# Kernel optimization log

Hardware: AMD Instinct MI355X
Metric: run time of the kernel (lower is better)

Reference implementation:

```python
import jax, jax.numpy as jnp
import numpy as np

N_STATES = 8
LBW = 128          # look_back_window == seq_len L (required by the einsum)
PRED_W = 16        # prediction_window
C = 16             # look_back_channel_dim
B = 512
LOG2PI = float(np.log(2.0 * np.pi))


def setup_inputs() -> dict:
    key = jax.random.key(0)
    k0, k1, k2, k3, k4 = jax.random.split(key, 5)
    emissions = jax.random.normal(k0, (B, LBW, C), jnp.float32)
    transition_matrix = jax.random.normal(k1, (N_STATES, N_STATES), jnp.float32)
    initial_distribution = jax.random.normal(k2, (N_STATES,), jnp.float32)
    means = jax.random.normal(k3, (N_STATES, C), jnp.float32)
    covar_chol = jnp.tile(jnp.eye(C, dtype=jnp.float32)[None], (N_STATES, 1, 1))
    W = jax.random.normal(k4, (N_STATES, LBW, C, C), jnp.float32) * 0.01
    return {"emissions": emissions, "transition_matrix": transition_matrix,
            "initial_distribution": initial_distribution, "means": means,
            "covar_chol": covar_chol, "W": W}


def reference(emissions, transition_matrix, initial_distribution, means, covar_chol, W):
    Bs, L, Cc = emissions.shape
    S = means.shape[0]
    lbw = W.shape[1]

    # --- positive-definite covariances from Cholesky factors (exp on diagonal) ---
    d = jnp.diagonal(covar_chol, axis1=-2, axis2=-1)                 # (S, C)
    chol = jnp.tril(covar_chol, -1) + jax.vmap(jnp.diag)(jnp.exp(d)) # (S, C, C)
    covar = chol @ jnp.swapaxes(chol, -1, -2) + 1e-6 * jnp.eye(Cc, dtype=emissions.dtype)
    prec = jnp.linalg.inv(covar)                                     # (S, C, C)
    Lc = jnp.linalg.cholesky(covar)
    logdet = 2.0 * jnp.sum(jnp.log(jnp.diagonal(Lc, axis1=-2, axis2=-1)), axis=-1)  # (S,)

    # --- per-step Gaussian log-likelihood with linear AR mean ---
    # causal zero-padded history: window f, element l = padded[f + l]
    padded = jnp.concatenate([jnp.zeros_like(emissions), emissions], axis=1)  # (B, 2L, C)
    idx = jnp.arange(L)[:, None] + jnp.arange(L)[None, :]                     # (L, L)
    inputs = padded[:, idx, :]                                                # (B, L, L, C)
    ar = jnp.einsum('bflc,slcd->bsfd', inputs, W)                             # (B, S, L, C)
    diff = emissions[:, None] - (ar + means[None, :, None])                   # (B, S, L, C)
    quad = jnp.einsum('bslc,scd,bsld->bsl', diff, prec, diff)                 # (B, S, L)
    emis_ll = -0.5 * (quad + logdet[None, :, None] + Cc * LOG2PI)
    emis_ll = jnp.transpose(emis_ll, (0, 2, 1))                               # (B, L, S)

    # --- HMM forward algorithm (log-space scan over time) ---
    log_trans = jnp.log(jax.nn.softmax(transition_matrix, axis=1) + 1e-8)     # (S, S)
    la0 = jnp.log(jax.nn.softmax(initial_distribution)) + emis_ll[:, 0]       # (B, S)

    def step(la, e_t):
        la = jax.nn.logsumexp(la[:, :, None] + log_trans[None], axis=1) + e_t
        return la, None

    la_last, _ = jax.lax.scan(step, la0, jnp.transpose(emis_ll[:, 1:], (1, 0, 2)))

    trans = jax.nn.softmax(transition_matrix, axis=1)
    state = jnp.argmax(la_last, axis=1)                                       # (B,)
    buf = emissions[:, -lbw:]                                                 # (B, lbw, C)
    preds = []
    for _ in range(PRED_W):
        state = jnp.argmax(trans[state], axis=1)
        pred = jnp.einsum('blc,blcd->bd', buf, W[state]) + means[state]       # (B, C)
        preds.append(pred)
        buf = jnp.concatenate([buf[:, 1:], pred[:, None]], axis=1)
    return jnp.stack(preds, axis=1)                                           # (B, PRED_W, C)
```

## Files before the change

kernel.cpp:

```cpp
#include <hip/hip_runtime.h>
#include <hip/hip_bf16.h>

#define LOG2PI_F 1.8378770664093453f
#define LOG2E_F  1.44269504f

typedef float f32x4 __attribute__((ext_vector_type(4)));
typedef short s16x8 __attribute__((ext_vector_type(8)));
typedef unsigned short u16;

#define OFF_PREC   0
#define OFF_LOGDET 2048
#define OFF_LTR    2064
#define OFF_LINI   2128
#define OFF_CHAIN  2144
#define OFF_CNT    2272
#define OFF_PERM   2304
#define OFF_ELL    8192
#define OFF_WT     532480

__device__ inline u16 f2bf(float x) {
  union { float f; unsigned u; } v; v.f = x;
  unsigned r = v.u + 0x7fffu + ((v.u >> 16) & 1u);
  return (u16)(r >> 16);
}

__device__ inline float fexp2(float x) {
#if __has_builtin(__builtin_amdgcn_exp2f)
  return __builtin_amdgcn_exp2f(x);
#else
  return exp2f(x);
#endif
}
__device__ inline float flog2(float x) {
#if __has_builtin(__builtin_amdgcn_logf)
  return __builtin_amdgcn_logf(x);
#else
  return log2f(x);
#endif
}

__global__ __launch_bounds__(256) void prep_wt_kernel(const float* __restrict__ tmat,
                                                      const float* __restrict__ initd,
                                                      const float* __restrict__ cc,
                                                      const float* __restrict__ W,
                                                      float* __restrict__ ws) {
  __shared__ float Ls[8][16][16];
  __shared__ float tmp[256];
  int t = threadIdx.x;

  if (blockIdx.x < 1024) {
    u16* Wt = (u16*)(ws + OFF_WT);
    int sl = blockIdx.x;
    tmp[t] = W[sl * 256 + t];
    __syncthreads();
    int d = t >> 4, c = t & 15;
    Wt[sl * 256 + t] = f2bf(tmp[c * 16 + d]);
    return;
  }

  float* prec   = ws + OFF_PREC;
  float* logdet = ws + OFF_LOGDET;
  float* ltr    = ws + OFF_LTR;
  float* lini   = ws + OFF_LINI;
  int*   chain  = (int*)(ws + OFF_CHAIN);

  if (t < 128) {
    int s = t >> 4, i = t & 15;
    const float* c0 = cc + s * 256 + i * 16;
    for (int j = 0; j < 16; ++j) {
      float v = c0[j];
      Ls[s][i][j] = (i > j) ? v : (i == j ? expf(v) : 0.f);
    }
  } else if (t < 136) {
    int s = t - 128;
    float ld = 0.f;
    for (int i = 0; i < 16; ++i) ld += cc[s * 256 + i * 17];
    logdet[s] = 2.f * ld;
  } else if (t == 136) {
    float m = -1e30f;
    for (int i = 0; i < 8; ++i) m = fmaxf(m, initd[i]);
    float sum = 0.f;
    for (int i = 0; i < 8; ++i) sum += expf(initd[i] - m);
    float lsum = logf(sum);
    for (int i = 0; i < 8; ++i) lini[i] = (initd[i] - m - lsum) * LOG2E_F;
  } else if (t == 137) {
    int nxt[8];
    for (int i = 0; i < 8; ++i) {
      float best = -1e30f; int bi = 0;
      for (int j = 0; j < 8; ++j) {
        float v = tmat[i * 8 + j];
        if (v > best) { best = v; bi = j; }
      }
      nxt[i] = bi;
    }
    for (int s0 = 0; s0 < 8; ++s0) {
      int c = s0;
      for (int k = 0; k < 16; ++k) { c = nxt[c]; chain[s0 * 16 + k] = c; }
    }
  } else if (t == 138) {
    int* cnt = (int*)(ws + OFF_CNT);
    for (int i = 0; i < 8; ++i) cnt[i] = 0;
  } else if (t >= 144 && t < 152) {
    int i = t - 144;
    float m = -1e30f;
    for (int j = 0; j < 8; ++j) m = fmaxf(m, tmat[i * 8 + j]);
    float sum = 0.f;
    for (int j = 0; j < 8; ++j) sum += expf(tmat[i * 8 + j] - m);
    for (int j = 0; j < 8; ++j)
      ltr[i * 8 + j] = logf(expf(tmat[i * 8 + j] - m) / sum + 1e-8f) * LOG2E_F;
  }
  __syncthreads();
  if (t < 128) {
    int s = t >> 4, col = t & 15;
    float y[16], x[16];
#pragma unroll
    for (int i = 0; i < 16; ++i) {
      float v = (i == col) ? 1.f : 0.f;
#pragma unroll
      for (int k = 0; k < 16; ++k) if (k < i) v -= Ls[s][i][k] * y[k];
      y[i] = v / Ls[s][i][i];
    }
#pragma unroll
    for (int i = 15; i >= 0; --i) {
      float v = y[i];
#pragma unroll
      for (int k = 0; k < 16; ++k) if (k > i) v -= Ls[s][k][i] * x[k];
      x[i] = v / Ls[s][i][i];
    }
#pragma unroll
    for (int i = 0; i < 16; ++i) prec[s * 256 + i * 16 + col] = x[i];
  }
}

__global__ __launch_bounds__(512, 4) void emis_kernel(const float* __restrict__ emis,
                                                      const float* __restrict__ means,
                                                      float* __restrict__ ws) {
  const float* prec   = ws + OFF_PREC;
  const float* logdet = ws + OFF_LOGDET;
  const u16* Wt = (const u16*)(ws + OFF_WT);
  float* ell = ws + OFF_ELL;

  int sp = blockIdx.x & 3;
  int bg = blockIdx.x >> 2;
  int s0 = sp * 2;
  int bb0 = bg * 4;
  int tid = threadIdx.x;

  __shared__ __align__(16) char smem[40960];
  char* pbase = smem;
  float* dlf = (float*)smem;
  const s16x8 zero8 = {0, 0, 0, 0, 0, 0, 0, 0};

  for (int i = tid; i < 1024; i += 512)
    *(s16x8*)(pbase + (i >> 8) * 8192 + (i & 255) * 16) = zero8;
  for (int i = tid; i < 1024; i += 512) {
    int g = i >> 8, erow = (i >> 1) & 127, h2 = i & 1;
    const f32x4* src = (const f32x4*)(emis + (size_t)(bb0 + g) * 2048 + erow * 16 + h2 * 8);
    f32x4 v0 = src[0], v1 = src[1];
    s16x8 pk;
#pragma unroll
    for (int c = 0; c < 4; ++c) { pk[c] = (short)f2bf(v0[c]); pk[c + 4] = (short)f2bf(v1[c]); }
    int row = 128 + erow;
    int off = ((row << 5) + (h2 << 4)) ^ (((row >> 2) & 3) << 4);
    *(s16x8*)(pbase + g * 8192 + off) = pk;
  }
  __syncthreads();

  int wave = tid >> 6, lane = tid & 63;
  int mt = (wave < 4) ? wave : 11 - wave;
  int rc = lane & 15;
  int h  = (lane >> 4) & 1;
  int dl = lane >> 5;
  int hh = h << 4;
  int kst = 56 - 8 * mt;
  int r0 = mt * 16 + rc + dl;

  const u16* Bp0 = Wt + ((size_t)((s0 * 128 + dl) * 16 + rc) * 16) + h * 8 + (size_t)kst * 512;
  const u16* Bp1 = Bp0 + 32768;

  f32x4 acc[2][4] = {};
  s16x8 w0 = *(const s16x8*)Bp0, w1 = *(const s16x8*)Bp1;
  for (int kk = kst; kk < 64; ++kk) {
    s16x8 n0, n1;
    if (kk < 63) { n0 = *(const s16x8*)(Bp0 + 512); n1 = *(const s16x8*)(Bp1 + 512); }
    Bp0 += 512; Bp1 += 512;
    int row = r0 + 2 * kk;
    const char* pa = pbase + (((row << 5) + hh) ^ (((row >> 2) & 3) << 4));
#pragma unroll
    for (int g = 0; g < 4; ++g) {
      s16x8 a = *(const s16x8*)(pa + g * 8192);
      acc[0][g] = __builtin_amdgcn_mfma_f32_16x16x32_bf16(a, w0, acc[0][g], 0, 0, 0);
      acc[1][g] = __builtin_amdgcn_mfma_f32_16x16x32_bf16(a, w1, acc[1][g], 0, 0, 0);
    }
    w0 = n0; w1 = n1;
  }

  int hi = (lane >> 4) & 3;
  float ev[4][4];
#pragma unroll
  for (int g = 0; g < 4; ++g)
#pragma unroll
    for (int r = 0; r < 4; ++r)
      ev[g][r] = emis[(size_t)(bb0 + g) * 2048 + (mt * 16 + hi * 4 + r) * 16 + rc];

  __syncthreads();

#pragma unroll
  for (int s = 0; s < 2; ++s) {
    float mn = means[(s0 + s) * 16 + rc];
#pragma unroll
    for (int g = 0; g < 4; ++g) {
#pragma unroll
      for (int r = 0; r < 4; ++r) {
        int f = mt * 16 + hi * 4 + r;
        dlf[(g * 128 + f) * 20 + rc] = ev[g][r] - acc[s][g][r] - mn;
      }
    }
    __syncthreads();
    const float* P = prec + (s0 + s) * 256;
    float c2 = -0.72134752f * (logdet[s0 + s] + 16.f * LOG2PI_F);
    {
      int g = tid >> 7, f = tid & 127;
      float dv[16];
#pragma unroll
      for (int c = 0; c < 4; ++c)
        *(f32x4*)&dv[c * 4] = *(const f32x4*)&dlf[(g * 128 + f) * 20 + c * 4];
      float qq = 0.f;
#pragma unroll
      for (int c = 0; c < 16; ++c) {
        float tsum = 0.5f * P[c * 16 + c] * dv[c];
#pragma unroll
        for (int d2 = 0; d2 < 16; ++d2)
          if (d2 > c) tsum = fmaf(P[c * 16 + d2], dv[d2], tsum);
        qq = fmaf(dv[c], tsum, qq);
      }
      ell[((size_t)(bb0 + g) * 8 + s0 + s) * 128 + f] = fmaf(-2.f * 0.72134752f, qq, c2);
    }
    if (s == 0) __syncthreads();
  }
}

__global__ __launch_bounds__(256) void fwd_kernel(float* __restrict__ ws) {
  const float* ell  = ws + OFF_ELL;
  const float* ltr  = ws + OFF_LTR;
  const float* lini = ws + OFF_LINI;
  int* cnt  = (int*)(ws + OFF_CNT);
  int* perm = (int*)(ws + OFF_PERM);

  __shared__ float leaf[8192];
  __shared__ float lvl[4096];
  __shared__ float ebuf[1024];
  __shared__ float LTs[64];
  __shared__ float redv[8];

  int b = blockIdx.x, tid = threadIdx.x;

  *(f32x4*)&ebuf[tid * 4] = *(const f32x4*)(ell + (size_t)b * 1024 + tid * 4);
  if (tid < 64) LTs[tid] = ltr[tid];
  __syncthreads();

  for (int t = tid; t < 8192; t += 256) {
    int m = t >> 6, i = (t >> 3) & 7, j = t & 7;
    float v;
    if (m < 127) v = LTs[i * 8 + j] + ebuf[j * 128 + (m + 1)];
    else         v = (i == j) ? 0.f : -1e30f;
    leaf[t] = v;
  }
  __syncthreads();

  float* src = leaf;
  float* dst = lvl;
  int nm = 64;
  for (int level = 0; level < 7; ++level) {
    for (int t = tid; t < nm * 64; t += 256) {
      int p = t >> 6, i = (t >> 3) & 7, j = t & 7;
      const float* Ma = src + (p * 2) * 64 + i * 8;
      const float* Mb = src + (p * 2 + 1) * 64 + j;
      float sv[8];
#pragma unroll
      for (int k = 0; k < 8; ++k) sv[k] = Ma[k] + Mb[k * 8];
      float m01 = fmaxf(sv[0], sv[1]), m23 = fmaxf(sv[2], sv[3]);
      float m45 = fmaxf(sv[4], sv[5]), m67 = fmaxf(sv[6], sv[7]);
      float m = fmaxf(fmaxf(m01, m23), fmaxf(m45, m67));
      float sum = ((fexp2(sv[0] - m) + fexp2(sv[1] - m))
                 + (fexp2(sv[2] - m) + fexp2(sv[3] - m)))
                + ((fexp2(sv[4] - m) + fexp2(sv[5] - m))
                 + (fexp2(sv[6] - m) + fexp2(sv[7] - m)));
      dst[p * 64 + i * 8 + j] = m + flog2(sum);
    }
    __syncthreads();
    float* tswap = src; src = dst; dst = tswap;
    nm >>= 1;
  }

  if (tid < 8) {
    int s = tid;
    float sv[8];
#pragma unroll
    for (int i = 0; i < 8; ++i)
      sv[i] = lini[i] + ebuf[i * 128] + src[i * 8 + s];
    float m01 = fmaxf(sv[0], sv[1]), m23 = fmaxf(sv[2], sv[3]);
    float m45 = fmaxf(sv[4], sv[5]), m67 = fmaxf(sv[6], sv[7]);
    float m = fmaxf(fmaxf(m01, m23), fmaxf(m45, m67));
    float sum = ((fexp2(sv[0] - m) + fexp2(sv[1] - m))
               + (fexp2(sv[2] - m) + fexp2(sv[3] - m)))
              + ((fexp2(sv[4] - m) + fexp2(sv[5] - m))
               + (fexp2(sv[6] - m) + fexp2(sv[7] - m)));
    redv[s] = m + flog2(sum);
  }
  __syncthreads();
  if (tid == 0) {
    float best = -1e30f; int bi = 0;
#pragma unroll
    for (int i = 0; i < 8; ++i) {
      float o = redv[i];
      if (o > best) { best = o; bi = i; }
    }
    int pos = atomicAdd(&cnt[bi], 1);
    perm[bi * 512 + pos] = b;
  }
}

__global__ __launch_bounds__(512, 2) void pred_kernel(const float* __restrict__ emis,
                                                      const float* __restrict__ means,
                                                      float* __restrict__ ws,
                                                      float* __restrict__ out) {
  const int* chain = (const int*)(ws + OFF_CHAIN);
  const int* cnt   = (const int*)(ws + OFF_CNT);
  const int* perm  = (const int*)(ws + OFF_PERM);
  const u16* Wt = (const u16*)(ws + OFF_WT);

  __shared__ u16 buf[16][128][16];
  __shared__ float part[8][64][4];
  __shared__ float ms[8][16];
  __shared__ int bid[16];

  int bucket = blockIdx.x >> 5, slot = blockIdx.x & 31;
  int nb = cnt[bucket];
  int base = slot * 16;
  if (base >= nb) return;
  int tid = threadIdx.x;
  char* pb = (char*)&buf[0][0][0];

  if (tid < 16) {
    int idx = base + tid;
    bid[tid] = perm[bucket * 512 + (idx < nb ? idx : base)];
  } else if (tid >= 128 && tid < 256) {
    int t2 = tid - 128;
    ms[t2 >> 4][t2 & 15] = means[t2];
  }
  __syncthreads();

  for (int i = tid; i < 2048; i += 512) {
    int b = i >> 7, row = i & 127;
    const f32x4* sp = (const f32x4*)(emis + (size_t)bid[b] * 2048 + row * 16);
    f32x4 v0 = sp[0], v1 = sp[1], v2 = sp[2], v3 = sp[3];
    s16x8 p0, p1;
#pragma unroll
    for (int j = 0; j < 4; ++j) {
      p0[j] = (short)f2bf(v0[j]); p0[4 + j] = (short)f2bf(v1[j]);
      p1[j] = (short)f2bf(v2[j]); p1[4 + j] = (short)f2bf(v3[j]);
    }
    int xo = (b & 7) << 4;
    int bse = b * 4096 + row * 32;
    *(s16x8*)(pb + (bse ^ xo)) = p0;
    *(s16x8*)(pb + ((bse + 16) ^ xo)) = p1;
  }
  __syncthreads();

  int wave = tid >> 6, lane = tid & 63;
  int rc = lane & 15;
  int q  = lane >> 4;
  int h  = q & 1;
  int dl = q >> 1;
  int axor = (rc & 7) << 4;
  const int* mychain = chain + bucket * 16;
  int b_own = q * 4 + (wave & 3);
  int bown_base = b_own * 4096;
  int bown_xor = (b_own & 7) << 4;

  float outv[16];
  int start = 0;
#pragma unroll
  for (int k = 0; k < 16; ++k) {
    int st = mychain[k];
    const u16* Bb = Wt + ((size_t)((st * 128 + dl) * 16 + rc) * 16) + h * 8;
    f32x4 accA = {0.f, 0.f, 0.f, 0.f}, accB = {0.f, 0.f, 0.f, 0.f};
#pragma unroll
    for (int t2 = 0; t2 < 4; ++t2) {
      int kkA = wave * 8 + t2 * 2, kkB = kkA + 1;
      s16x8 wA = *(const s16x8*)(Bb + (size_t)kkA * 512);
      s16x8 wB2 = *(const s16x8*)(Bb + (size_t)kkB * 512);
      int rowA = (start + kkA * 2 + dl) & 127;
      int rowB = (start + kkB * 2 + dl) & 127;
      s16x8 aA = *(const s16x8*)(pb + ((rc * 4096 + rowA * 32 + h * 16) ^ axor));
      s16x8 aB = *(const s16x8*)(pb + ((rc * 4096 + rowB * 32 + h * 16) ^ axor));
      accA = __builtin_amdgcn_mfma_f32_16x16x32_bf16(aA, wA, accA, 0, 0, 0);
      accB = __builtin_amdgcn_mfma_f32_16x16x32_bf16(aB, wB2, accB, 0, 0, 0);
    }
    f32x4 acc = accA + accB;
    *(f32x4*)&part[wave][lane][0] = acc;
    __syncthreads();
    if (wave < 4) {
      f32x4 cs = (*(f32x4*)&part[0][lane][0] + *(f32x4*)&part[1][lane][0])
               + (*(f32x4*)&part[2][lane][0] + *(f32x4*)&part[3][lane][0]);
      f32x4 cs2 = (*(f32x4*)&part[4][lane][0] + *(f32x4*)&part[5][lane][0])
                + (*(f32x4*)&part[6][lane][0] + *(f32x4*)&part[7][lane][0]);
      cs = cs + cs2;
      float vown = (wave & 3) == 0 ? cs[0] : (wave & 3) == 1 ? cs[1]
                 : (wave & 3) == 2 ? cs[2] : cs[3];
      float o = vown + ms[st][rc];
      outv[k] = o;
      *(u16*)(pb + ((bown_base + start * 32 + rc * 2) ^ bown_xor)) = f2bf(o);
    }
    __syncthreads();
    start = (start + 1) & 127;
  }
  if (wave < 4 && base + b_own < nb) {
    float* op = out + (size_t)bid[b_own] * 256 + rc;
#pragma unroll
    for (int k = 0; k < 16; ++k) op[k * 16] = outv[k];
  }
}

extern "C" void kernel_launch(void* const* d_in, const int* in_sizes, int n_in,
                              void* d_out, int out_size, void* d_ws, size_t ws_size,
                              hipStream_t stream) {
  const float* emis  = (const float*)d_in[0];
  const float* tmat  = (const float*)d_in[1];
  const float* initd = (const float*)d_in[2];
  const float* means = (const float*)d_in[3];
  const float* cc    = (const float*)d_in[4];
  const float* W     = (const float*)d_in[5];
  float* ws  = (float*)d_ws;
  float* out = (float*)d_out;

  hipLaunchKernelGGL(prep_wt_kernel, dim3(1025), dim3(256), 0, stream, tmat, initd, cc, W, ws);
  hipLaunchKernelGGL(emis_kernel, dim3(512), dim3(512), 0, stream, emis, means, ws);
  hipLaunchKernelGGL(fwd_kernel, dim3(512), dim3(256), 0, stream, ws);
  hipLaunchKernelGGL(pred_kernel, dim3(256), dim3(512), 0, stream, emis, means, ws, out);
}
```

Measured before the change: 74.06 us.

## Switch forward tree reduction to scaled linear-space matmul; halve pred_kernel block size

The forward algorithm's log-space tree of 8x8 log-sum-exp matrix products becomes linear-space products. Leaves are exponentiated once after subtracting a per-step max, and each product is renormalised by its max across the wave. This removes the exp/log work per element at each of the seven levels. Separately, pred_kernel moves from 8 waves to 4, so each wave does twice the MFMA chain and the cross-wave reduction shrinks. Risks are precision loss from rescaling only by the per-product max and less parallelism in the prediction stage.

Result: slower. 82.13 us (+10.9%).

```diff
diff --git a/kernel.cpp b/kernel.cpp
--- a/kernel.cpp
+++ b/kernel.cpp
@@ -29,13 +29,6 @@
   return __builtin_amdgcn_exp2f(x);
 #else
   return exp2f(x);
-#endif
-}
-__device__ inline float flog2(float x) {
-#if __has_builtin(__builtin_amdgcn_logf)
-  return __builtin_amdgcn_logf(x);
-#else
-  return log2f(x);
 #endif
 }
 
@@ -251,19 +244,32 @@
   __shared__ float lvl[4096];
   __shared__ float ebuf[1024];
   __shared__ float LTs[64];
+  __shared__ float kmax[128];
   __shared__ float redv[8];
 
   int b = blockIdx.x, tid = threadIdx.x;
 
   *(f32x4*)&ebuf[tid * 4] = *(const f32x4*)(ell + (size_t)b * 1024 + tid * 4);
   if (tid < 64) LTs[tid] = ltr[tid];
+  __syncthreads();
+
+  if (tid < 128) {
+    int m = tid;
+    float mx = 0.f;
+    if (m < 127) {
+      mx = -1e30f;
+#pragma unroll
+      for (int j = 0; j < 8; ++j) mx = fmaxf(mx, ebuf[j * 128 + m + 1]);
+    }
+    kmax[m] = mx;
+  }
   __syncthreads();
 
   for (int t = tid; t < 8192; t += 256) {
     int m = t >> 6, i = (t >> 3) & 7, j = t & 7;
     float v;
-    if (m < 127) v = LTs[i * 8 + j] + ebuf[j * 128 + (m + 1)];
-    else         v = (i == j) ? 0.f : -1e30f;
+    if (m < 127) v = fexp2(LTs[i * 8 + j] + ebuf[j * 128 + (m + 1)] - kmax[m]);
+    else         v = (i == j) ? 1.f : 0.f;
     leaf[t] = v;
   }
   __syncthreads();
@@ -276,17 +282,13 @@
       int p = t >> 6, i = (t >> 3) & 7, j = t & 7;
       const float* Ma = src + (p * 2) * 64 + i * 8;
       const float* Mb = src + (p * 2 + 1) * 64 + j;
-      float sv[8];
-#pragma unroll
-      for (int k = 0; k < 8; ++k) sv[k] = Ma[k] + Mb[k * 8];
-      float m01 = fmaxf(sv[0], sv[1]), m23 = fmaxf(sv[2], sv[3]);
-      float m45 = fmaxf(sv[4], sv[5]), m67 = fmaxf(sv[6], sv[7]);
-      float m = fmaxf(fmaxf(m01, m23), fmaxf(m45, m67));
-      float sum = ((fexp2(sv[0] - m) + fexp2(sv[1] - m))
-                 + (fexp2(sv[2] - m) + fexp2(sv[3] - m)))
-                + ((fexp2(sv[4] - m) + fexp2(sv[5] - m))
-                 + (fexp2(sv[6] - m) + fexp2(sv[7] - m)));
-      dst[p * 64 + i * 8 + j] = m + flog2(sum);
+      float sum = 0.f;
+#pragma unroll
+      for (int k = 0; k < 8; ++k) sum = fmaf(Ma[k], Mb[k * 8], sum);
+      float mx = sum;
+#pragma unroll
+      for (int o2 = 32; o2; o2 >>= 1) mx = fmaxf(mx, __shfl_xor(mx, o2));
+      dst[t] = sum / mx;
     }
     __syncthreads();
     float* tswap = src; src = dst; dst = tswap;
@@ -295,18 +297,14 @@
 
   if (tid < 8) {
     int s = tid;
-    float sv[8];
+    float k0 = -1e30f;
+#pragma unroll
+    for (int i = 0; i < 8; ++i) k0 = fmaxf(k0, lini[i] + ebuf[i * 128]);
+    float v = 0.f;
 #pragma unroll
     for (int i = 0; i < 8; ++i)
-      sv[i] = lini[i] + ebuf[i * 128] + src[i * 8 + s];
-    float m01 = fmaxf(sv[0], sv[1]), m23 = fmaxf(sv[2], sv[3]);
-    float m45 = fmaxf(sv[4], sv[5]), m67 = fmaxf(sv[6], sv[7]);
-    float m = fmaxf(fmaxf(m01, m23), fmaxf(m45, m67));
-    float sum = ((fexp2(sv[0] - m) + fexp2(sv[1] - m))
-               + (fexp2(sv[2] - m) + fexp2(sv[3] - m)))
-              + ((fexp2(sv[4] - m) + fexp2(sv[5] - m))
-               + (fexp2(sv[6] - m) + fexp2(sv[7] - m)));
-    redv[s] = m + flog2(sum);
+      v = fmaf(fexp2(lini[i] + ebuf[i * 128] - k0), src[i * 8 + s], v);
+    redv[s] = v;
   }
   __syncthreads();
   if (tid == 0) {
@@ -321,7 +319,7 @@
   }
 }
 
-__global__ __launch_bounds__(512, 2) void pred_kernel(const float* __restrict__ emis,
+__global__ __launch_bounds__(256, 2) void pred_kernel(const float* __restrict__ emis,
                                                       const float* __restrict__ means,
                                                       float* __restrict__ ws,
                                                       float* __restrict__ out) {
@@ -331,7 +329,7 @@
   const u16* Wt = (const u16*)(ws + OFF_WT);
 
   __shared__ u16 buf[16][128][16];
-  __shared__ float part[8][64][4];
+  __shared__ float part[4][64][4];
   __shared__ float ms[8][16];
   __shared__ int bid[16];
 
@@ -351,7 +349,7 @@
   }
   __syncthreads();
 
-  for (int i = tid; i < 2048; i += 512) {
+  for (int i = tid; i < 2048; i += 256) {
     int b = i >> 7, row = i & 127;
     const f32x4* sp = (const f32x4*)(emis + (size_t)bid[b] * 2048 + row * 16);
     f32x4 v0 = sp[0], v1 = sp[1], v2 = sp[2], v3 = sp[3];
@@ -375,7 +373,7 @@
   int dl = q >> 1;
   int axor = (rc & 7) << 4;
   const int* mychain = chain + bucket * 16;
-  int b_own = q * 4 + (wave & 3);
+  int b_own = q * 4 + wave;
   int bown_base = b_own * 4096;
   int bown_xor = (b_own & 7) << 4;
 
@@ -387,8 +385,8 @@
     const u16* Bb = Wt + ((size_t)((st * 128 + dl) * 16 + rc) * 16) + h * 8;
     f32x4 accA = {0.f, 0.f, 0.f, 0.f}, accB = {0.f, 0.f, 0.f, 0.f};
 #pragma unroll
-    for (int t2 = 0; t2 < 4; ++t2) {
-      int kkA = wave * 8 + t2 * 2, kkB = kkA + 1;
+    for (int t2 = 0; t2 < 8; ++t2) {
+      int kkA = wave * 16 + t2 * 2, kkB = kkA + 1;
       s16x8 wA = *(const s16x8*)(Bb + (size_t)kkA * 512);
       s16x8 wB2 = *(const s16x8*)(Bb + (size_t)kkB * 512);
       int rowA = (start + kkA * 2 + dl) & 127;
@@ -401,22 +399,16 @@
     f32x4 acc = accA + accB;
     *(f32x4*)&part[wave][lane][0] = acc;
     __syncthreads();
-    if (wave < 4) {
-      f32x4 cs = (*(f32x4*)&part[0][lane][0] + *(f32x4*)&part[1][lane][0])
-               + (*(f32x4*)&part[2][lane][0] + *(f32x4*)&part[3][lane][0]);
-      f32x4 cs2 = (*(f32x4*)&part[4][lane][0] + *(f32x4*)&part[5][lane][0])
-                + (*(f32x4*)&part[6][lane][0] + *(f32x4*)&part[7][lane][0]);
-      cs = cs + cs2;
-      float vown = (wave & 3) == 0 ? cs[0] : (wave & 3) == 1 ? cs[1]
-                 : (wave & 3) == 2 ? cs[2] : cs[3];
-      float o = vown + ms[st][rc];
-      outv[k] = o;
-      *(u16*)(pb + ((bown_base + start * 32 + rc * 2) ^ bown_xor)) = f2bf(o);
-    }
+    f32x4 cs = (*(f32x4*)&part[0][lane][0] + *(f32x4*)&part[1][lane][0])
+             + (*(f32x4*)&part[2][lane][0] + *(f32x4*)&part[3][lane][0]);
+    float vown = wave == 0 ? cs[0] : wave == 1 ? cs[1] : wave == 2 ? cs[2] : cs[3];
+    float o = vown + ms[st][rc];
+    outv[k] = o;
+    *(u16*)(pb + ((bown_base + start * 32 + rc * 2) ^ bown_xor)) = f2bf(o);
     __syncthreads();
     start = (start + 1) & 127;
   }
-  if (wave < 4 && base + b_own < nb) {
+  if (base + b_own < nb) {
     float* op = out + (size_t)bid[b_own] * 256 + rc;
 #pragma unroll
     for (int k = 0; k < 16; ++k) op[k * 16] = outv[k];
@@ -438,5 +430,5 @@
   hipLaunchKernelGGL(prep_wt_kernel, dim3(1025), dim3(256), 0, stream, tmat, initd, cc, W, ws);
   hipLaunchKernelGGL(emis_kernel, dim3(512), dim3(512), 0, stream, emis, means, ws);
   hipLaunchKernelGGL(fwd_kernel, dim3(512), dim3(256), 0, stream, ws);
-  hipLaunchKernelGGL(pred_kernel, dim3(256), dim3(512), 0, stream, emis, means, ws, out);
-}
+  hipLaunchKernelGGL(pred_kernel, dim3(256), dim3(256), 0, stream, emis, means, ws, out);
+}
```
